# Performance work log

Measured on AMD Instinct MI355X. Metric: run time of the kernel, lower is better.

The kernel has to match this reference:

```python
import jax, jax.numpy as jnp
import numpy as np

EPS = 1e-12

def _l2norm(x):
    # F.normalize(x, p=2, dim=1) applied on [B*N, D] == normalize last dim of [B, N, D]
    return x / jnp.maximum(jnp.linalg.norm(x, axis=-1, keepdims=True), EPS)

def setup_inputs() -> dict:
    key = jax.random.key(0)
    k1, k2 = jax.random.split(key)
    B, N, D = 128, 64, 128  # batch_size, num_epoch, feature_dim
    feat_k = jax.random.normal(k1, (B, N, D), dtype=jnp.float32)
    feat_q = jax.random.normal(k2, (B, N, D), dtype=jnp.float32)
    return {"feat_k": feat_k, "feat_q": feat_q}

def reference(feat_k, feat_q):
    B, N, D = feat_k.shape
    fk = _l2norm(feat_k)                       # [B, N, D]
    fq = jax.lax.stop_gradient(_l2norm(feat_q))  # sampler branch is no_grad

    # Dense pairwise similarities, as in the original einsum('ijk,mnk->ijnm')
    logits = jnp.einsum('ijk,mnk->ijnm', fk, fk)  # [B, N, N, B]
    sim    = jnp.einsum('ijk,mnk->ijnm', fq, fq)  # [B, N, N, B]

    el = jnp.exp(logits)

    # mask[i, j, n, m] = (m == i):
    #   pos[i, j] = sum_n exp(logits[i, j, n, i])
    pos = jnp.einsum('ijni->ij', el)              # diagonal over (i, m), summed over n

    #   neg[i, j] = sum_{n, m != i} exp(logits[i, j, n, m]) * sim[i, j, n, m]
    prod = el * sim
    neg = prod.sum(axis=(2, 3)) - jnp.einsum('ijni->ij', prod)

    loss = jnp.mean(-jnp.log(pos / (pos + neg)))
    return loss
```

## Files before the change

kernel.cpp:

```cpp
#include <hip/hip_runtime.h>
#include <stdint.h>

#define ROWS 8192
#define D    128
#define NSB  32
#define BM   256
#define BN   64
#define NT   4
#define NBLK (NSB * (NSB + 1) / 2)
#define SQRT_LOG2E 1.2011224087864498f

typedef __bf16 bf16x8 __attribute__((ext_vector_type(8)));
typedef float  f32x4  __attribute__((ext_vector_type(4)));

typedef const __attribute__((address_space(1))) uint32_t guint;
typedef __attribute__((address_space(3))) uint32_t luint;

__device__ __forceinline__ void gload_lds16(const void* g, void* l) {
    __builtin_amdgcn_global_load_lds((guint*)g, (luint*)l, 16, 0, 0);
}

__device__ __forceinline__ ushort f2bf(float f) {
    union { float f; uint32_t u; } x; x.f = f;
    uint32_t r = x.u + 0x7FFFu + ((x.u >> 16) & 1u);
    return (ushort)(r >> 16);
}

__global__ __launch_bounds__(256) void k_norm(
    const float* __restrict__ fk, const float* __restrict__ fq,
    ushort* __restrict__ fkn, ushort* __restrict__ fqn)
{
    int gw = (blockIdx.x * 256 + threadIdx.x) >> 6;
    int l  = threadIdx.x & 63;
    const float* src; ushort* dst; int r; float scale;
    if (gw < ROWS) { src = fk; dst = fkn; r = gw; scale = SQRT_LOG2E; }
    else           { src = fq; dst = fqn; r = gw - ROWS; scale = 1.0f; }
    float2 v = *reinterpret_cast<const float2*>(&src[r * D + l * 2]);
    float ss = v.x * v.x + v.y * v.y;
    #pragma unroll
    for (int m = 1; m < 64; m <<= 1) ss += __shfl_xor(ss, m, 64);
    float inv = scale / fmaxf(sqrtf(ss), 1e-12f);
    ushort2 o; o.x = f2bf(v.x * inv); o.y = f2bf(v.y * inv);
    *reinterpret_cast<ushort2*>(&dst[r * D + l * 2]) = o;
}

__global__ __launch_bounds__(512, 4) void k_gram(
    const ushort* __restrict__ fkn, const ushort* __restrict__ fqn,
    float* __restrict__ pneg, float* __restrict__ ppos)
{
    __shared__ ushort lds[2][2 * BN * D];
    const int b = blockIdx.x;
    int I, J;
    if (b < NSB) { I = b; J = b; }
    else {
        int x = b - NSB, i = 0;
        while (x >= NSB - 1 - i) { x -= NSB - 1 - i; ++i; }
        I = i; J = i + 1 + x;
    }
    const bool isdiag = (I == J);
    const int w = threadIdx.x >> 6;
    const int l = threadIdx.x & 63;
    const int lrow = l >> 4, lcol = l & 15;
    const int r0 = I * BM;
    const int c0 = J * BM;

    int off[2];
    #pragma unroll
    for (int i = 0; i < 2; ++i) {
        int L = w * 128 + i * 64 + l;
        int row = L >> 4, slot = L & 15;
        off[i] = row * 256 + (slot ^ (row & 7)) * 16;
    }

    auto issue_stage = [&](int buf, int cbase) {
        const char* fkb = (const char*)fkn + (size_t)cbase * 256;
        const char* fqb = (const char*)fqn + (size_t)cbase * 256;
        ushort* lk = &lds[buf][w * 1024];
        ushort* lq = &lds[buf][BN * D + w * 1024];
        gload_lds16(fkb + off[0], lk);
        gload_lds16(fkb + off[1], lk + 512);
        gload_lds16(fqb + off[0], lq);
        gload_lds16(fqb + off[1], lq + 512);
    };

    issue_stage(0, c0);

    bf16x8 ak[2][4], aq[2][4];
    #pragma unroll
    for (int rg = 0; rg < 2; ++rg) {
        int arow = r0 + w * 32 + rg * 16 + lcol;
        #pragma unroll
        for (int ks = 0; ks < 4; ++ks) {
            ak[rg][ks] = *reinterpret_cast<const bf16x8*>(fkn + arow * D + ks * 32 + lrow * 8);
            aq[rg][ks] = *reinterpret_cast<const bf16x8*>(fqn + arow * D + ks * 32 + lrow * 8);
        }
    }

    const int diagc = (r0 + w * 32) & ~63;

    float accn[2][4] = {};
    float colacc[16] = {};

    __syncthreads();

    #pragma unroll
    for (int t = 0; t < NT; ++t) {
        const int cur = t & 1;
        if (t + 1 < NT) issue_stage(cur ^ 1, c0 + (t + 1) * BN);
        const int cbase = c0 + t * BN;
        const bool dtile = isdiag && (cbase == diagc);
        const ushort* bkb = &lds[cur][0];
        const ushort* bqb = &lds[cur][BN * D];
        #pragma unroll
        for (int cc = 0; cc < 4; ++cc) {
            int brow = cc * 16 + lcol;
            bf16x8 bk[4], bq[4];
            #pragma unroll
            for (int ks = 0; ks < 4; ++ks) {
                int slot = (ks * 4 + lrow) ^ (brow & 7);
                bk[ks] = *reinterpret_cast<const bf16x8*>(bkb + brow * 128 + slot * 8);
                bq[ks] = *reinterpret_cast<const bf16x8*>(bqb + brow * 128 + slot * 8);
            }
            f32x4 sk0 = {0,0,0,0}, sk1 = {0,0,0,0}, sq0 = {0,0,0,0}, sq1 = {0,0,0,0};
            __builtin_amdgcn_s_setprio(1);
            #pragma unroll
            for (int ks = 0; ks < 4; ++ks) {
                sk0 = __builtin_amdgcn_mfma_f32_16x16x32_bf16(ak[0][ks], bk[ks], sk0, 0, 0, 0);
                sk1 = __builtin_amdgcn_mfma_f32_16x16x32_bf16(ak[1][ks], bk[ks], sk1, 0, 0, 0);
                sq0 = __builtin_amdgcn_mfma_f32_16x16x32_bf16(aq[0][ks], bq[ks], sq0, 0, 0, 0);
                sq1 = __builtin_amdgcn_mfma_f32_16x16x32_bf16(aq[1][ks], bq[ks], sq1, 0, 0, 0);
            }
            __builtin_amdgcn_s_setprio(0);
            if (dtile) {
                #pragma unroll
                for (int e = 0; e < 4; ++e) {
                    colacc[0 * 4 + e] += __builtin_exp2f(sk0[e]);
                    colacc[1 * 4 + e] += __builtin_exp2f(sk1[e]);
                }
            } else {
                float psum = 0.f;
                #pragma unroll
                for (int e = 0; e < 4; ++e) {
                    float p0 = __builtin_exp2f(sk0[e]) * sq0[e];
                    float p1 = __builtin_exp2f(sk1[e]) * sq1[e];
                    accn[0][e] += p0;
                    accn[1][e] += p1;
                    psum += p0 + p1;
                }
                if (!isdiag) colacc[t * 4 + cc] += psum;
            }
        }
        __syncthreads();
    }

    #pragma unroll
    for (int m = 1; m <= 8; m <<= 1) {
        #pragma unroll
        for (int rg = 0; rg < 2; ++rg)
            #pragma unroll
            for (int e = 0; e < 4; ++e)
                accn[rg][e] += __shfl_xor(accn[rg][e], m, 64);
    }
    if (isdiag) {
        #pragma unroll
        for (int m = 1; m <= 8; m <<= 1)
            #pragma unroll
            for (int i = 0; i < 8; ++i)
                colacc[i] += __shfl_xor(colacc[i], m, 64);
    }
    if (lcol == 0) {
        #pragma unroll
        for (int rg = 0; rg < 2; ++rg)
            #pragma unroll
            for (int e = 0; e < 4; ++e) {
                int gr = r0 + w * 32 + rg * 16 + lrow * 4 + e;
                pneg[J * ROWS + gr] = accn[rg][e];
                if (isdiag) ppos[gr] = colacc[rg * 4 + e];
            }
    }

    if (!isdiag) {
        #pragma unroll
        for (int i = 0; i < 16; ++i) {
            colacc[i] += __shfl_xor(colacc[i], 16, 64);
            colacc[i] += __shfl_xor(colacc[i], 32, 64);
        }
        float* colbuf = (float*)&lds[0][0];
        if (l < 16) {
            #pragma unroll
            for (int i = 0; i < 16; ++i)
                colbuf[w * 256 + (i >> 2) * 64 + (i & 3) * 16 + l] = colacc[i];
        }
        __syncthreads();
        if (threadIdx.x < 256) {
            int c = threadIdx.x;
            float s = 0.f;
            #pragma unroll
            for (int ww = 0; ww < 8; ++ww) s += colbuf[ww * 256 + c];
            pneg[I * ROWS + c0 + c] = s;
        }
    }
}

__global__ __launch_bounds__(256) void k_loss1(
    const float* __restrict__ pneg, const float* __restrict__ ppos,
    float* __restrict__ bsum)
{
    int r = blockIdx.x * 256 + threadIdx.x;
    float pos = ppos[r];
    float neg = 0.f;
    #pragma unroll
    for (int p = 0; p < NSB; ++p) neg += pneg[p * ROWS + r];
    float s = log1pf(neg / pos);
    #pragma unroll
    for (int m = 1; m < 64; m <<= 1) s += __shfl_xor(s, m, 64);
    __shared__ float red[4];
    if ((threadIdx.x & 63) == 0) red[threadIdx.x >> 6] = s;
    __syncthreads();
    if (threadIdx.x == 0) bsum[blockIdx.x] = red[0] + red[1] + red[2] + red[3];
}

__global__ void k_loss2(const float* __restrict__ bsum, float* __restrict__ out)
{
    int l = threadIdx.x;
    float s = (l < 32) ? bsum[l] : 0.f;
    #pragma unroll
    for (int m = 1; m < 64; m <<= 1) s += __shfl_xor(s, m, 64);
    if (l == 0) out[0] = s * (1.0f / ROWS);
}

extern "C" void kernel_launch(void* const* d_in, const int* in_sizes, int n_in,
                              void* d_out, int out_size, void* d_ws, size_t ws_size,
                              hipStream_t stream)
{
    const float* fk = (const float*)d_in[0];
    const float* fq = (const float*)d_in[1];
    ushort* fkn = (ushort*)d_ws;
    ushort* fqn = fkn + ROWS * D;
    float*  pneg = (float*)(fqn + ROWS * D);
    float*  ppos = pneg + NSB * ROWS;
    float*  bsum = ppos + ROWS;

    k_norm<<<(2 * ROWS) / 4, 256, 0, stream>>>(fk, fq, fkn, fqn);
    k_gram<<<NBLK, 512, 0, stream>>>(fkn, fqn, pneg, ppos);
    k_loss1<<<32, 256, 0, stream>>>(pneg, ppos, bsum);
    k_loss2<<<1, 64, 0, stream>>>(bsum, (float*)d_out);
}
```

Before: 56.95 us.

## Rebalance symmetric Gram work into 512 equal column-tile blocks

```diff
diff --git a/kernel.cpp b/kernel.cpp
--- a/kernel.cpp
+++ b/kernel.cpp
@@ -4,10 +4,8 @@
 #define ROWS 8192
 #define D    128
 #define NSB  32
-#define BM   256
 #define BN   64
-#define NT   4
-#define NBLK (NSB * (NSB + 1) / 2)
+#define NSLOT 64
 #define SQRT_LOG2E 1.2011224087864498f
 
 typedef __bf16 bf16x8 __attribute__((ext_vector_type(8)));
@@ -49,20 +47,23 @@
     float* __restrict__ pneg, float* __restrict__ ppos)
 {
     __shared__ ushort lds[2][2 * BN * D];
-    const int b = blockIdx.x;
-    int I, J;
-    if (b < NSB) { I = b; J = b; }
-    else {
-        int x = b - NSB, i = 0;
-        while (x >= NSB - 1 - i) { x -= NSB - 1 - i; ++i; }
-        I = i; J = i + 1 + x;
-    }
-    const bool isdiag = (I == J);
+    int b = blockIdx.x;
+    int I = 0;
+    #pragma unroll 1
+    for (; I < 31; ++I) {
+        int nI = (I < 16) ? (31 - I) : (32 - I);
+        if (b < nI) break;
+        b -= nI;
+    }
+    const int k = b;
+    const int nt = (I < 16 && k < 4) ? 5 : 4;
+    const int tstart = (I < 16) ? (k < 4 ? k * 5 : 20 + (k - 4) * 4) : k * 4;
+    const int ct0 = I * 4 + tstart;
+    const int r0 = I * 256;
+
     const int w = threadIdx.x >> 6;
     const int l = threadIdx.x & 63;
     const int lrow = l >> 4, lcol = l & 15;
-    const int r0 = I * BM;
-    const int c0 = J * BM;
 
     int off[2];
     #pragma unroll
@@ -83,7 +84,7 @@
         gload_lds16(fqb + off[1], lq + 512);
     };
 
-    issue_stage(0, c0);
+    issue_stage(0, ct0 * 64);
 
     bf16x8 ak[2][4], aq[2][4];
     #pragma unroll
@@ -96,108 +97,135 @@
         }
     }
 
-    const int diagc = (r0 + w * 32) & ~63;
+    const int diagct = (r0 + w * 32) >> 6;
+    const bool haspos = (tstart == 0);
 
     float accn[2][4] = {};
-    float colacc[16] = {};
+    float colacc[5][4] = {};
+    float posacc[2][4] = {};
 
     __syncthreads();
 
     #pragma unroll
-    for (int t = 0; t < NT; ++t) {
-        const int cur = t & 1;
-        if (t + 1 < NT) issue_stage(cur ^ 1, c0 + (t + 1) * BN);
-        const int cbase = c0 + t * BN;
-        const bool dtile = isdiag && (cbase == diagc);
-        const ushort* bkb = &lds[cur][0];
-        const ushort* bqb = &lds[cur][BN * D];
-        #pragma unroll
-        for (int cc = 0; cc < 4; ++cc) {
-            int brow = cc * 16 + lcol;
-            bf16x8 bk[4], bq[4];
-            #pragma unroll
-            for (int ks = 0; ks < 4; ++ks) {
-                int slot = (ks * 4 + lrow) ^ (brow & 7);
-                bk[ks] = *reinterpret_cast<const bf16x8*>(bkb + brow * 128 + slot * 8);
-                bq[ks] = *reinterpret_cast<const bf16x8*>(bqb + brow * 128 + slot * 8);
-            }
-            f32x4 sk0 = {0,0,0,0}, sk1 = {0,0,0,0}, sq0 = {0,0,0,0}, sq1 = {0,0,0,0};
-            __builtin_amdgcn_s_setprio(1);
-            #pragma unroll
-            for (int ks = 0; ks < 4; ++ks) {
-                sk0 = __builtin_amdgcn_mfma_f32_16x16x32_bf16(ak[0][ks], bk[ks], sk0, 0, 0, 0);
-                sk1 = __builtin_amdgcn_mfma_f32_16x16x32_bf16(ak[1][ks], bk[ks], sk1, 0, 0, 0);
-                sq0 = __builtin_amdgcn_mfma_f32_16x16x32_bf16(aq[0][ks], bq[ks], sq0, 0, 0, 0);
-                sq1 = __builtin_amdgcn_mfma_f32_16x16x32_bf16(aq[1][ks], bq[ks], sq1, 0, 0, 0);
-            }
-            __builtin_amdgcn_s_setprio(0);
-            if (dtile) {
-                #pragma unroll
-                for (int e = 0; e < 4; ++e) {
-                    colacc[0 * 4 + e] += __builtin_exp2f(sk0[e]);
-                    colacc[1 * 4 + e] += __builtin_exp2f(sk1[e]);
+    for (int t = 0; t < 5; ++t) {
+        if (t < nt) {
+            const int cur = t & 1;
+            if (t + 1 < nt) issue_stage(cur ^ 1, (ct0 + t + 1) * 64);
+            const int ct = ct0 + t;
+            const bool dtile  = (ct == diagct);
+            const bool indiag = (ct < 4 * I + 4);
+            const ushort* bkb = &lds[cur][0];
+            const ushort* bqb = &lds[cur][BN * D];
+            #pragma unroll
+            for (int cc = 0; cc < 4; ++cc) {
+                int brow = cc * 16 + lcol;
+                bf16x8 bk[4], bq[4];
+                #pragma unroll
+                for (int ks = 0; ks < 4; ++ks) {
+                    int slot = (ks * 4 + lrow) ^ (brow & 7);
+                    bk[ks] = *reinterpret_cast<const bf16x8*>(bkb + brow * 128 + slot * 8);
+                    bq[ks] = *reinterpret_cast<const bf16x8*>(bqb + brow * 128 + slot * 8);
                 }
-            } else {
-                float psum = 0.f;
-                #pragma unroll
-                for (int e = 0; e < 4; ++e) {
-                    float p0 = __builtin_exp2f(sk0[e]) * sq0[e];
-                    float p1 = __builtin_exp2f(sk1[e]) * sq1[e];
-                    accn[0][e] += p0;
-                    accn[1][e] += p1;
-                    psum += p0 + p1;
+                f32x4 sk0 = {0,0,0,0}, sk1 = {0,0,0,0}, sq0 = {0,0,0,0}, sq1 = {0,0,0,0};
+                __builtin_amdgcn_s_setprio(1);
+                #pragma unroll
+                for (int ks = 0; ks < 4; ++ks) {
+                    sk0 = __builtin_amdgcn_mfma_f32_16x16x32_bf16(ak[0][ks], bk[ks], sk0, 0, 0, 0);
+                    sk1 = __builtin_amdgcn_mfma_f32_16x16x32_bf16(ak[1][ks], bk[ks], sk1, 0, 0, 0);
+                    sq0 = __builtin_amdgcn_mfma_f32_16x16x32_bf16(aq[0][ks], bq[ks], sq0, 0, 0, 0);
+                    sq1 = __builtin_amdgcn_mfma_f32_16x16x32_bf16(aq[1][ks], bq[ks], sq1, 0, 0, 0);
                 }
-                if (!isdiag) colacc[t * 4 + cc] += psum;
-            }
-        }
-        __syncthreads();
-    }
-
-    #pragma unroll
-    for (int m = 1; m <= 8; m <<= 1) {
+                __builtin_amdgcn_s_setprio(0);
+                if (dtile) {
+                    #pragma unroll
+                    for (int e = 0; e < 4; ++e) {
+                        posacc[0][e] += __builtin_exp2f(sk0[e]);
+                        posacc[1][e] += __builtin_exp2f(sk1[e]);
+                    }
+                } else {
+                    float psum = 0.f;
+                    #pragma unroll
+                    for (int e = 0; e < 4; ++e) {
+                        float p0 = __builtin_exp2f(sk0[e]) * sq0[e];
+                        float p1 = __builtin_exp2f(sk1[e]) * sq1[e];
+                        accn[0][e] += p0;
+                        accn[1][e] += p1;
+                        psum += p0 + p1;
+                    }
+                    if (!indiag) colacc[t][cc] += psum;
+                }
+            }
+            const int J = ct >> 2;
+            if (t == nt - 1 || ((ct + 1) >> 2) != J) {
+                #pragma unroll
+                for (int m = 1; m <= 8; m <<= 1)
+                    #pragma unroll
+                    for (int rg = 0; rg < 2; ++rg)
+                        #pragma unroll
+                        for (int e = 0; e < 4; ++e)
+                            accn[rg][e] += __shfl_xor(accn[rg][e], m, 64);
+                const int h = (ct0 <= 4 * J) ? 0 : 1;
+                if (lcol == 0) {
+                    #pragma unroll
+                    for (int rg = 0; rg < 2; ++rg)
+                        #pragma unroll
+                        for (int e = 0; e < 4; ++e) {
+                            int gr = r0 + w * 32 + rg * 16 + lrow * 4 + e;
+                            pneg[(2 * J + h) * ROWS + gr] = accn[rg][e];
+                        }
+                    }
+                #pragma unroll
+                for (int rg = 0; rg < 2; ++rg)
+                    #pragma unroll
+                    for (int e = 0; e < 4; ++e) accn[rg][e] = 0.f;
+            }
+            __syncthreads();
+        }
+    }
+
+    #pragma unroll
+    for (int m = 1; m <= 8; m <<= 1)
         #pragma unroll
         for (int rg = 0; rg < 2; ++rg)
             #pragma unroll
             for (int e = 0; e < 4; ++e)
-                accn[rg][e] += __shfl_xor(accn[rg][e], m, 64);
-    }
-    if (isdiag) {
-        #pragma unroll
-        for (int m = 1; m <= 8; m <<= 1)
-            #pragma unroll
-            for (int i = 0; i < 8; ++i)
-                colacc[i] += __shfl_xor(colacc[i], m, 64);
-    }
-    if (lcol == 0) {
+                posacc[rg][e] += __shfl_xor(posacc[rg][e], m, 64);
+    if (haspos && lcol == 0) {
         #pragma unroll
         for (int rg = 0; rg < 2; ++rg)
             #pragma unroll
             for (int e = 0; e < 4; ++e) {
                 int gr = r0 + w * 32 + rg * 16 + lrow * 4 + e;
-                pneg[J * ROWS + gr] = accn[rg][e];
-                if (isdiag) ppos[gr] = colacc[rg * 4 + e];
-            }
-    }
-
-    if (!isdiag) {
-        #pragma unroll
-        for (int i = 0; i < 16; ++i) {
-            colacc[i] += __shfl_xor(colacc[i], 16, 64);
-            colacc[i] += __shfl_xor(colacc[i], 32, 64);
-        }
-        float* colbuf = (float*)&lds[0][0];
-        if (l < 16) {
-            #pragma unroll
-            for (int i = 0; i < 16; ++i)
-                colbuf[w * 256 + (i >> 2) * 64 + (i & 3) * 16 + l] = colacc[i];
-        }
-        __syncthreads();
-        if (threadIdx.x < 256) {
-            int c = threadIdx.x;
-            float s = 0.f;
-            #pragma unroll
-            for (int ww = 0; ww < 8; ++ww) s += colbuf[ww * 256 + c];
-            pneg[I * ROWS + c0 + c] = s;
+                ppos[gr] = posacc[rg][e];
+            }
+    }
+
+    #pragma unroll
+    for (int i = 0; i < 5; ++i)
+        #pragma unroll
+        for (int cc = 0; cc < 4; ++cc) {
+            colacc[i][cc] += __shfl_xor(colacc[i][cc], 16, 64);
+            colacc[i][cc] += __shfl_xor(colacc[i][cc], 32, 64);
+        }
+    float* colbuf = (float*)&lds[0][0];
+    if (l < 16) {
+        #pragma unroll
+        for (int i = 0; i < 5; ++i)
+            #pragma unroll
+            for (int cc = 0; cc < 4; ++cc)
+                colbuf[w * 320 + i * 64 + cc * 16 + l] = colacc[i][cc];
+    }
+    __syncthreads();
+    {
+        int cl = threadIdx.x;
+        if (cl < nt * 64) {
+            int ct = ct0 + (cl >> 6);
+            if (ct >= 4 * I + 4) {
+                float s = 0.f;
+                #pragma unroll
+                for (int ww = 0; ww < 8; ++ww) s += colbuf[ww * 320 + cl];
+                pneg[I * ROWS + ct * 64 + (cl & 63)] = s;
+            }
         }
     }
 }
@@ -210,7 +238,7 @@
     float pos = ppos[r];
     float neg = 0.f;
     #pragma unroll
-    for (int p = 0; p < NSB; ++p) neg += pneg[p * ROWS + r];
+    for (int p = 0; p < NSLOT; ++p) neg += pneg[p * ROWS + r];
     float s = log1pf(neg / pos);
     #pragma unroll
     for (int m = 1; m < 64; m <<= 1) s += __shfl_xor(s, m, 64);
@@ -238,11 +266,12 @@
     ushort* fkn = (ushort*)d_ws;
     ushort* fqn = fkn + ROWS * D;
     float*  pneg = (float*)(fqn + ROWS * D);
-    float*  ppos = pneg + NSB * ROWS;
+    float*  ppos = pneg + NSLOT * ROWS;
     float*  bsum = ppos + ROWS;
 
+    hipMemsetAsync(pneg, 0, (size_t)NSLOT * ROWS * sizeof(float), stream);
     k_norm<<<(2 * ROWS) / 4, 256, 0, stream>>>(fk, fq, fkn, fqn);
-    k_gram<<<NBLK, 512, 0, stream>>>(fkn, fqn, pneg, ppos);
+    k_gram<<<512, 512, 0, stream>>>(fkn, fqn, pneg, ppos);
     k_loss1<<<32, 256, 0, stream>>>(pneg, ppos, bsum);
     k_loss2<<<1, 64, 0, stream>>>(bsum, (float*)d_out);
 }
```

New measurement: 74.93 us. +31.6%, slower.
